# Kernel tuning notes

Measured on AMD Instinct MI355X. Metric: run time of the kernel, lower is better.

## Reference

```python
import jax, jax.numpy as jnp
import numpy as np

B, T, N_EMBD, HEAD = 4, 4096, 1024, 64


def setup_inputs() -> dict:
    key = jax.random.key(0)
    kx, kk, kq, kv = jax.random.split(key, 4)
    x = jax.random.normal(kx, (B, T, N_EMBD), dtype=jnp.float32)
    s = 1.0 / np.sqrt(N_EMBD)  # init scale so activations stay O(1)
    Wk = jax.random.normal(kk, (N_EMBD, HEAD), dtype=jnp.float32) * s
    Wq = jax.random.normal(kq, (N_EMBD, HEAD), dtype=jnp.float32) * s
    Wv = jax.random.normal(kv, (N_EMBD, HEAD), dtype=jnp.float32) * s
    return {"x": x, "Wk": Wk, "Wq": Wq, "Wv": Wv}


def reference(x, Wk, Wq, Wv):
    Bd, Td, C = x.shape
    k = jnp.einsum('btc,ch->bth', x, Wk)
    q = jnp.einsum('btc,ch->bth', x, Wq)
    v = jnp.einsum('btc,ch->bth', x, Wv)
    # scores scaled by C**-0.5 where C = n_embd (as in the source, not head_size)
    w = jnp.einsum('bth,bsh->bts', q, k) * (C ** -0.5)
    causal = jnp.tril(jnp.ones((Td, Td), dtype=bool))  # [T, T]
    w = jnp.where(causal, w, -jnp.inf)
    w = jax.nn.softmax(w, axis=-1)
    out = jnp.einsum('bts,bsh->bth', w, v)  # [B, T, head_size]
    return out
```

## Files before the change

kernel.cpp:

```cpp
#include <hip/hip_runtime.h>
#include <cmath>

#define NB 4
#define NT 4096
#define NC 1024
#define NH 64
#define SCALE 0.03125f
#define MFIX 3.0f
#define LOG2E 1.4426950408889634f
#define NSPLIT 12

typedef __attribute__((ext_vector_type(8))) short v8s;
typedef __attribute__((ext_vector_type(4))) float f32x4;

static __device__ __forceinline__ ushort f2bf(float x) {
    union { float f; uint u; } c; c.f = x;
    return (ushort)((c.u + 0x7FFF + ((c.u >> 16) & 1)) >> 16);
}
static __device__ __forceinline__ float bf2f(ushort h) {
    union { uint u; float f; } c; c.u = (uint)h << 16;
    return c.f;
}
static __device__ __forceinline__ uint pk2bf(float hi_f, float lo_f) {
    uint uh = __float_as_uint(hi_f) + 0x8000u;
    uint ul = __float_as_uint(lo_f) + 0x8000u;
    return __builtin_amdgcn_perm(uh, ul, 0x07060302u);
}

__global__ __launch_bounds__(256) void prep_kernel(
    const float* __restrict__ Wk, const float* __restrict__ Wq,
    const float* __restrict__ Wv, ushort* __restrict__ Wb)
{
    const int g    = blockIdx.x * 256 + threadIdx.x;
    const int lane = g & 63;
    const int kc   = (g >> 6) & 31;
    const int nt   = g >> 11;
    const int n    = nt * 16 + (lane & 15);
    const float* W = (n < 64) ? Wq : (n < 128) ? Wk : Wv;
    const int col  = n & 63;
    const int k0   = kc * 32 + ((lane >> 4) << 3);
    ushort t8[8];
    #pragma unroll
    for (int j = 0; j < 8; ++j)
        t8[j] = f2bf(W[(k0 + j) * 64 + col]);
    *(uint4*)(Wb + (size_t)g * 8) = *(const uint4*)t8;
}

#define PPAD 72

__global__ __launch_bounds__(256) void proj_kernel(
    const float* __restrict__ x, const ushort* __restrict__ Wb,
    ushort* __restrict__ qpack, ushort* __restrict__ kpack,
    ushort* __restrict__ vpack)
{
    __shared__ __align__(16) ushort As[2][16 * PPAD];
    __shared__ __align__(16) ushort Cs[16][200];

    const int tid  = threadIdx.x;
    const int w    = tid >> 6;
    const int lane = tid & 63;
    const int ln   = lane & 15;
    const int quad = lane >> 4;
    const long r0  = (long)blockIdx.x * 16;

    const int arow = tid >> 4, acol = (tid & 15) * 4;
    const float* xs = x + (r0 + arow) * NC + acol;

    const ushort* wb0 = Wb + (size_t)(w * 3 + 0) * 16384 + lane * 8;
    const ushort* wb1 = Wb + (size_t)(w * 3 + 1) * 16384 + lane * 8;
    const ushort* wb2 = Wb + (size_t)(w * 3 + 2) * 16384 + lane * 8;

    f32x4 acc[3];
    #pragma unroll
    for (int nt = 0; nt < 3; ++nt) acc[nt] = (f32x4){0.f,0.f,0.f,0.f};

    float4 f0 = *(const float4*)(xs);
    v8s b[3][2];
    b[0][0] = *(const v8s*)(wb0);       b[0][1] = *(const v8s*)(wb0 + 512);
    b[1][0] = *(const v8s*)(wb1);       b[1][1] = *(const v8s*)(wb1 + 512);
    b[2][0] = *(const v8s*)(wb2);       b[2][1] = *(const v8s*)(wb2 + 512);
    {
        uint2 p = { pk2bf(f0.y, f0.x), pk2bf(f0.w, f0.z) };
        *(uint2*)(&As[0][arow * PPAD + acol]) = p;
    }
    __syncthreads();

    int buf = 0;
    #pragma unroll
    for (int it = 0; it < 16; ++it) {
        float4 g0;
        v8s nb[3][2];
        if (it < 15) {
            const int k1 = (it + 1) * 64;
            g0 = *(const float4*)(xs + k1);
            const int off = (it + 1) * 1024;
            nb[0][0] = *(const v8s*)(wb0 + off); nb[0][1] = *(const v8s*)(wb0 + off + 512);
            nb[1][0] = *(const v8s*)(wb1 + off); nb[1][1] = *(const v8s*)(wb1 + off + 512);
            nb[2][0] = *(const v8s*)(wb2 + off); nb[2][1] = *(const v8s*)(wb2 + off + 512);
        }

        const ushort* ap = &As[buf][ln * PPAD + quad * 8];
        v8s a0 = *(const v8s*)(ap);
        v8s a1 = *(const v8s*)(ap + 32);
        #pragma unroll
        for (int nt = 0; nt < 3; ++nt) {
            acc[nt] = __builtin_amdgcn_mfma_f32_16x16x32_bf16(a0, b[nt][0], acc[nt], 0, 0, 0);
            acc[nt] = __builtin_amdgcn_mfma_f32_16x16x32_bf16(a1, b[nt][1], acc[nt], 0, 0, 0);
        }

        if (it < 15) {
            uint2 p = { pk2bf(g0.y, g0.x), pk2bf(g0.w, g0.z) };
            *(uint2*)(&As[buf ^ 1][arow * PPAD + acol]) = p;
            #pragma unroll
            for (int nt = 0; nt < 3; ++nt) {
                b[nt][0] = nb[nt][0];
                b[nt][1] = nb[nt][1];
            }
        }
        __syncthreads();
        buf ^= 1;
    }

    #pragma unroll
    for (int nt = 0; nt < 3; ++nt)
        #pragma unroll
        for (int r = 0; r < 4; ++r)
            Cs[quad * 4 + r][(w * 3 + nt) * 16 + ln] = f2bf(acc[nt][r]);
    __syncthreads();

    const int b_blk = (int)(r0 >> 12);
    const int t_loc = (int)(r0 & 4095);
    const int kt    = t_loc >> 6;
    const int qt16  = t_loc >> 4;
    const int kcb   = (t_loc >> 5) & 1;
    const int half  = (t_loc >> 4) & 1;

    if (tid < 128) {
        const int kc = tid >> 6, lp = tid & 63;
        const int lnp = lp & 15, qdp = lp >> 4;
        uint4 u = *(const uint4*)(&Cs[lnp][kc * 32 + qdp * 8]);
        size_t fid = ((size_t)(b_blk * 256 + qt16) * 2 + kc);
        *(uint4*)(qpack + fid * 512 + lp * 8) = u;
        const int td = tid >> 5, lp2 = tid & 31;
        const int ql = lp2 >> 4, lnv = lp2 & 15;
        ushort t8[8];
        #pragma unroll
        for (int j = 0; j < 8; ++j)
            t8[j] = Cs[ql * 8 + j][128 + td * 16 + lnv];
        size_t fv = ((size_t)(b_blk * 64 + kt) * 2 + kcb) * 4 + td;
        const int lane_g = (half * 2 + ql) * 16 + lnv;
        *(uint4*)(vpack + fv * 512 + lane_g * 8) = *(const uint4*)t8;
    } else {
        const int kc = (tid >> 6) & 1, lp = tid & 63;
        const int lnp = lp & 15, qdp = lp >> 4;
        uint4 u = *(const uint4*)(&Cs[lnp][64 + kc * 32 + qdp * 8]);
        size_t fid = ((size_t)(b_blk * 256 + qt16) * 2 + kc);
        *(uint4*)(kpack + fid * 512 + lp * 8) = u;
    }
}

#define LPAD 72

__global__ __launch_bounds__(256) void attn_kernel(
    const ushort* __restrict__ qpack, const ushort* __restrict__ kpack,
    const ushort* __restrict__ vpack, ushort* __restrict__ Op,
    float* __restrict__ Lp)
{
    __shared__ __align__(16) ushort Ps[4][32 * LPAD];

    const int id = blockIdx.x;
    const int qt = 31 - (id / 48);
    const int c  = (id % 48) >> 2;
    const int b  = id & 3;
    const int q0 = qt * 128;

    const int tid  = threadIdx.x;
    const int w    = tid >> 6;
    const int lane = tid & 63;
    const int ln   = lane & 15;
    const int quad = lane >> 4;
    const int qw0  = q0 + w * 32;
    const int qt16w = (qw0 >> 4);

    const ushort* qpb = qpack + (size_t)b * 256 * 2 * 512 + lane * 8;
    const ushort* kpb = kpack + (size_t)b * 64 * 8 * 512 + lane * 8;
    const ushort* vpb = vpack + (size_t)b * 64 * 8 * 512 + lane * 8;

    v8s qf[2][2];
    #pragma unroll
    for (int s = 0; s < 2; ++s) {
        qf[s][0] = *(const v8s*)(qpb + ((qt16w + s) * 2 + 0) * 512);
        qf[s][1] = *(const v8s*)(qpb + ((qt16w + s) * 2 + 1) * 512);
    }

    f32x4 o[2][4];
    #pragma unroll
    for (int s = 0; s < 2; ++s)
        #pragma unroll
        for (int td = 0; td < 4; ++td) o[s][td] = (f32x4){0.f,0.f,0.f,0.f};
    float l[2] = {0.f, 0.f};

    const int nkt   = 2 * qt + 2;
    const int cs    = (nkt + NSPLIT - 1) / NSPLIT;
    const int kt_lo = c * cs;
    const int kt_hi = min(nkt, kt_lo + cs);

    ushort* Pw = &Ps[w][0];

    for (int kt = kt_lo; kt < kt_hi; ++kt) {
        const ushort* kfb = kpb + (size_t)kt * 8 * 512;
        const ushort* vfb = vpb + (size_t)kt * 8 * 512;

        #pragma unroll
        for (int tk = 0; tk < 4; ++tk) {
            v8s kf0 = *(const v8s*)(kfb + (tk * 2 + 0) * 512);
            v8s kf1 = *(const v8s*)(kfb + (tk * 2 + 1) * 512);
            const int keybase = kt * 64 + tk * 16 + quad * 4;
            #pragma unroll
            for (int s = 0; s < 2; ++s) {
                f32x4 acc = (f32x4){0.f,0.f,0.f,0.f};
                acc = __builtin_amdgcn_mfma_f32_16x16x32_bf16(kf0, qf[s][0], acc, 0, 0, 0);
                acc = __builtin_amdgcn_mfma_f32_16x16x32_bf16(kf1, qf[s][1], acc, 0, 0, 0);
                const int qg = qw0 + s * 16 + ln;
                const bool needmask = (kt * 64 + 63) > (qw0 + s * 16);
                float p[4];
                #pragma unroll
                for (int r = 0; r < 4; ++r) {
                    float e = fmaf(acc[r], SCALE * LOG2E, -MFIX * LOG2E);
                    if (needmask && (keybase + r > qg)) e = -1e30f;
                    p[r] = __builtin_amdgcn_exp2f(e);
                    l[s] += p[r];
                }
                uint2 pw = { pk2bf(p[1], p[0]), pk2bf(p[3], p[2]) };
                *(uint2*)(&Pw[(s * 16 + ln) * LPAD + tk * 16 + quad * 4]) = pw;
            }
        }

        #pragma unroll
        for (int kc = 0; kc < 2; ++kc) {
            v8s vf[4];
            #pragma unroll
            for (int td = 0; td < 4; ++td)
                vf[td] = *(const v8s*)(vfb + (kc * 4 + td) * 512);
            #pragma unroll
            for (int s = 0; s < 2; ++s) {
                v8s pf = *(const v8s*)(&Pw[(s * 16 + ln) * LPAD + kc * 32 + quad * 8]);
                #pragma unroll
                for (int td = 0; td < 4; ++td)
                    o[s][td] = __builtin_amdgcn_mfma_f32_16x16x32_bf16(pf, vf[td], o[s][td], 0, 0, 0);
            }
        }
    }

    #pragma unroll
    for (int s = 0; s < 2; ++s) {
        l[s] += __shfl_xor(l[s], 16);
        l[s] += __shfl_xor(l[s], 32);
    }

    ushort* opc = Op + (size_t)c * NB * NT * NH + (size_t)b * NT * NH;
    float*  lpc = Lp + (size_t)c * NB * NT + (size_t)b * NT;
    #pragma unroll
    for (int s = 0; s < 2; ++s) {
        if (quad == 0) lpc[qw0 + s * 16 + ln] = l[s];
        #pragma unroll
        for (int r = 0; r < 4; ++r) {
            const int t = qw0 + s * 16 + quad * 4 + r;
            #pragma unroll
            for (int td = 0; td < 4; ++td)
                opc[(size_t)t * NH + td * 16 + ln] = f2bf(o[s][td][r]);
        }
    }
}

__global__ __launch_bounds__(256) void combine_kernel(
    const ushort* __restrict__ Op, const float* __restrict__ Lp,
    float* __restrict__ out)
{
    const size_t g4 = (size_t)blockIdx.x * 256 + threadIdx.x;
    const size_t h0 = (g4 & 15) * 4;
    const size_t bq = g4 >> 4;
    const size_t QN = (size_t)NB * NT;
    const size_t ON = QN * NH;
    float L = 0.f;
    float o0 = 0.f, o1 = 0.f, o2 = 0.f, o3 = 0.f;
    #pragma unroll
    for (int c = 0; c < NSPLIT; ++c) {
        L += Lp[(size_t)c * QN + bq];
        ushort4 u = *(const ushort4*)(Op + (size_t)c * ON + bq * NH + h0);
        o0 += bf2f(u.x); o1 += bf2f(u.y); o2 += bf2f(u.z); o3 += bf2f(u.w);
    }
    const float inv = 1.f / L;
    float4 r = { o0 * inv, o1 * inv, o2 * inv, o3 * inv };
    *(float4*)(out + bq * NH + h0) = r;
}

extern "C" void kernel_launch(void* const* d_in, const int* in_sizes, int n_in,
                              void* d_out, int out_size, void* d_ws, size_t ws_size,
                              hipStream_t stream)
{
    const float* x  = (const float*)d_in[0];
    const float* Wk = (const float*)d_in[1];
    const float* Wq = (const float*)d_in[2];
    const float* Wv = (const float*)d_in[3];
    float* out = (float*)d_out;

    char* wsb = (char*)d_ws;
    const size_t QE = (size_t)NB * NT * NH;
    ushort* qpack = (ushort*)wsb;
    ushort* kpack = qpack + QE;
    ushort* vpack = kpack + QE;
    ushort* Wb    = vpack + QE;
    ushort* Op    = (ushort*)(wsb + (8u << 20));
    float*  Lp    = (float*)(wsb + (40u << 20));

    prep_kernel<<<96, 256, 0, stream>>>(Wk, Wq, Wv, Wb);
    proj_kernel<<<NB * NT / 16, 256, 0, stream>>>(x, Wb, qpack, kpack, vpack);
    attn_kernel<<<32 * NSPLIT * NB, 256, 0, stream>>>(qpack, kpack, vpack, Op, Lp);
    combine_kernel<<<(int)(QE / 4 / 256), 256, 0, stream>>>(Op, Lp, out);
}
```

Baseline: 143.6 us.

## Double projection rows per block and store attention partials in fragment layout

The projection kernel now handles 32 rows per block instead of 16, so each loaded weight fragment feeds twice as many MFMAs and x loads are 8-wide. The attention kernel writes its partial outputs as packed bf16 in MFMA fragment order with vector stores, replacing scattered 2-byte stores. The combine kernel reads that fragment layout with vector loads and sums four L values at once. The trade-off is half as many projection blocks, which lowers parallelism, plus combine output writes that are now strided rather than float4.

```diff
diff --git a/kernel.cpp b/kernel.cpp
--- a/kernel.cpp
+++ b/kernel.cpp
@@ -9,6 +9,7 @@
 #define MFIX 3.0f
 #define LOG2E 1.4426950408889634f
 #define NSPLIT 12
+#define QE 1048576
 
 typedef __attribute__((ext_vector_type(8))) short v8s;
 typedef __attribute__((ext_vector_type(4))) float f32x4;
@@ -53,64 +54,73 @@
     ushort* __restrict__ qpack, ushort* __restrict__ kpack,
     ushort* __restrict__ vpack)
 {
-    __shared__ __align__(16) ushort As[2][16 * PPAD];
-    __shared__ __align__(16) ushort Cs[16][200];
+    __shared__ __align__(16) ushort As[2][32 * PPAD];
+    __shared__ __align__(16) ushort Cs[32][200];
 
     const int tid  = threadIdx.x;
     const int w    = tid >> 6;
     const int lane = tid & 63;
     const int ln   = lane & 15;
     const int quad = lane >> 4;
-    const long r0  = (long)blockIdx.x * 16;
-
-    const int arow = tid >> 4, acol = (tid & 15) * 4;
+    const long r0  = (long)blockIdx.x * 32;
+
+    const int arow = tid >> 3, acol = (tid & 7) * 8;
     const float* xs = x + (r0 + arow) * NC + acol;
 
     const ushort* wb0 = Wb + (size_t)(w * 3 + 0) * 16384 + lane * 8;
     const ushort* wb1 = Wb + (size_t)(w * 3 + 1) * 16384 + lane * 8;
     const ushort* wb2 = Wb + (size_t)(w * 3 + 2) * 16384 + lane * 8;
 
-    f32x4 acc[3];
-    #pragma unroll
-    for (int nt = 0; nt < 3; ++nt) acc[nt] = (f32x4){0.f,0.f,0.f,0.f};
+    f32x4 acc[2][3];
+    #pragma unroll
+    for (int s = 0; s < 2; ++s)
+        #pragma unroll
+        for (int nt = 0; nt < 3; ++nt) acc[s][nt] = (f32x4){0.f,0.f,0.f,0.f};
 
     float4 f0 = *(const float4*)(xs);
+    float4 f1 = *(const float4*)(xs + 4);
     v8s b[3][2];
     b[0][0] = *(const v8s*)(wb0);       b[0][1] = *(const v8s*)(wb0 + 512);
     b[1][0] = *(const v8s*)(wb1);       b[1][1] = *(const v8s*)(wb1 + 512);
     b[2][0] = *(const v8s*)(wb2);       b[2][1] = *(const v8s*)(wb2 + 512);
     {
-        uint2 p = { pk2bf(f0.y, f0.x), pk2bf(f0.w, f0.z) };
-        *(uint2*)(&As[0][arow * PPAD + acol]) = p;
+        uint4 p = { pk2bf(f0.y, f0.x), pk2bf(f0.w, f0.z),
+                    pk2bf(f1.y, f1.x), pk2bf(f1.w, f1.z) };
+        *(uint4*)(&As[0][arow * PPAD + acol]) = p;
     }
     __syncthreads();
 
     int buf = 0;
     #pragma unroll
     for (int it = 0; it < 16; ++it) {
-        float4 g0;
+        float4 g0, g1;
         v8s nb[3][2];
         if (it < 15) {
             const int k1 = (it + 1) * 64;
             g0 = *(const float4*)(xs + k1);
+            g1 = *(const float4*)(xs + k1 + 4);
             const int off = (it + 1) * 1024;
             nb[0][0] = *(const v8s*)(wb0 + off); nb[0][1] = *(const v8s*)(wb0 + off + 512);
             nb[1][0] = *(const v8s*)(wb1 + off); nb[1][1] = *(const v8s*)(wb1 + off + 512);
             nb[2][0] = *(const v8s*)(wb2 + off); nb[2][1] = *(const v8s*)(wb2 + off + 512);
         }
 
-        const ushort* ap = &As[buf][ln * PPAD + quad * 8];
-        v8s a0 = *(const v8s*)(ap);
-        v8s a1 = *(const v8s*)(ap + 32);
-        #pragma unroll
-        for (int nt = 0; nt < 3; ++nt) {
-            acc[nt] = __builtin_amdgcn_mfma_f32_16x16x32_bf16(a0, b[nt][0], acc[nt], 0, 0, 0);
-            acc[nt] = __builtin_amdgcn_mfma_f32_16x16x32_bf16(a1, b[nt][1], acc[nt], 0, 0, 0);
+        #pragma unroll
+        for (int s = 0; s < 2; ++s) {
+            const ushort* ap = &As[buf][(s * 16 + ln) * PPAD + quad * 8];
+            v8s a0 = *(const v8s*)(ap);
+            v8s a1 = *(const v8s*)(ap + 32);
+            #pragma unroll
+            for (int nt = 0; nt < 3; ++nt) {
+                acc[s][nt] = __builtin_amdgcn_mfma_f32_16x16x32_bf16(a0, b[nt][0], acc[s][nt], 0, 0, 0);
+                acc[s][nt] = __builtin_amdgcn_mfma_f32_16x16x32_bf16(a1, b[nt][1], acc[s][nt], 0, 0, 0);
+            }
         }
 
         if (it < 15) {
-            uint2 p = { pk2bf(g0.y, g0.x), pk2bf(g0.w, g0.z) };
-            *(uint2*)(&As[buf ^ 1][arow * PPAD + acol]) = p;
+            uint4 p = { pk2bf(g0.y, g0.x), pk2bf(g0.w, g0.z),
+                        pk2bf(g1.y, g1.x), pk2bf(g1.w, g1.z) };
+            *(uint4*)(&As[buf ^ 1][arow * PPAD + acol]) = p;
             #pragma unroll
             for (int nt = 0; nt < 3; ++nt) {
                 b[nt][0] = nb[nt][0];
@@ -122,40 +132,38 @@
     }
 
     #pragma unroll
-    for (int nt = 0; nt < 3; ++nt)
-        #pragma unroll
-        for (int r = 0; r < 4; ++r)
-            Cs[quad * 4 + r][(w * 3 + nt) * 16 + ln] = f2bf(acc[nt][r]);
+    for (int s = 0; s < 2; ++s)
+        #pragma unroll
+        for (int nt = 0; nt < 3; ++nt)
+            #pragma unroll
+            for (int r = 0; r < 4; ++r)
+                Cs[s * 16 + quad * 4 + r][(w * 3 + nt) * 16 + ln] = f2bf(acc[s][nt][r]);
     __syncthreads();
 
     const int b_blk = (int)(r0 >> 12);
     const int t_loc = (int)(r0 & 4095);
     const int kt    = t_loc >> 6;
-    const int qt16  = t_loc >> 4;
     const int kcb   = (t_loc >> 5) & 1;
-    const int half  = (t_loc >> 4) & 1;
-
-    if (tid < 128) {
-        const int kc = tid >> 6, lp = tid & 63;
+    const int qt16a = t_loc >> 4;
+
+    {
+        const int f = tid >> 6, sx = f >> 1, kc = f & 1, lp = tid & 63;
         const int lnp = lp & 15, qdp = lp >> 4;
-        uint4 u = *(const uint4*)(&Cs[lnp][kc * 32 + qdp * 8]);
-        size_t fid = ((size_t)(b_blk * 256 + qt16) * 2 + kc);
-        *(uint4*)(qpack + fid * 512 + lp * 8) = u;
-        const int td = tid >> 5, lp2 = tid & 31;
-        const int ql = lp2 >> 4, lnv = lp2 & 15;
+        const size_t fid = ((size_t)(b_blk * 256 + qt16a + sx) * 2 + kc);
+        uint4 uq = *(const uint4*)(&Cs[sx * 16 + lnp][kc * 32 + qdp * 8]);
+        *(uint4*)(qpack + fid * 512 + lp * 8) = uq;
+        uint4 uk = *(const uint4*)(&Cs[sx * 16 + lnp][64 + kc * 32 + qdp * 8]);
+        *(uint4*)(kpack + fid * 512 + lp * 8) = uk;
+    }
+    {
+        const int td = tid >> 6, lp = tid & 63;
+        const int lnv = lp & 15, qg = lp >> 4;
         ushort t8[8];
         #pragma unroll
         for (int j = 0; j < 8; ++j)
-            t8[j] = Cs[ql * 8 + j][128 + td * 16 + lnv];
-        size_t fv = ((size_t)(b_blk * 64 + kt) * 2 + kcb) * 4 + td;
-        const int lane_g = (half * 2 + ql) * 16 + lnv;
-        *(uint4*)(vpack + fv * 512 + lane_g * 8) = *(const uint4*)t8;
-    } else {
-        const int kc = (tid >> 6) & 1, lp = tid & 63;
-        const int lnp = lp & 15, qdp = lp >> 4;
-        uint4 u = *(const uint4*)(&Cs[lnp][64 + kc * 32 + qdp * 8]);
-        size_t fid = ((size_t)(b_blk * 256 + qt16) * 2 + kc);
-        *(uint4*)(kpack + fid * 512 + lp * 8) = u;
+            t8[j] = Cs[qg * 8 + j][128 + td * 16 + lnv];
+        const size_t fv = ((size_t)(b_blk * 64 + kt) * 2 + kcb) * 4 + td;
+        *(uint4*)(vpack + fv * 512 + lp * 8) = *(const uint4*)t8;
     }
 }
 
@@ -258,17 +266,16 @@
         l[s] += __shfl_xor(l[s], 32);
     }
 
-    ushort* opc = Op + (size_t)c * NB * NT * NH + (size_t)b * NT * NH;
-    float*  lpc = Lp + (size_t)c * NB * NT + (size_t)b * NT;
+    float* lpc = Lp + (size_t)c * NB * NT + (size_t)b * NT;
+    const size_t obase = (((size_t)c * NB + b) * 32 + qt) * 4 + w;
     #pragma unroll
     for (int s = 0; s < 2; ++s) {
         if (quad == 0) lpc[qw0 + s * 16 + ln] = l[s];
         #pragma unroll
-        for (int r = 0; r < 4; ++r) {
-            const int t = qw0 + s * 16 + quad * 4 + r;
-            #pragma unroll
-            for (int td = 0; td < 4; ++td)
-                opc[(size_t)t * NH + td * 16 + ln] = f2bf(o[s][td][r]);
+        for (int td = 0; td < 4; ++td) {
+            uint2 pw = { pk2bf(o[s][td][1], o[s][td][0]),
+                         pk2bf(o[s][td][3], o[s][td][2]) };
+            *(uint2*)(Op + (((obase * 2 + s) * 4 + td) * 256 + lane * 4)) = pw;
         }
     }
 }
@@ -277,22 +284,34 @@
     const ushort* __restrict__ Op, const float* __restrict__ Lp,
     float* __restrict__ out)
 {
-    const size_t g4 = (size_t)blockIdx.x * 256 + threadIdx.x;
-    const size_t h0 = (g4 & 15) * 4;
-    const size_t bq = g4 >> 4;
+    const uint g   = blockIdx.x * 256 + threadIdx.x;
+    const int lane = g & 63, ln = lane & 15, quad = lane >> 4;
+    const int td   = (g >> 6) & 3;
+    const int s    = (g >> 8) & 1;
+    const int w    = (g >> 9) & 3;
+    const int qt   = (g >> 11) & 31;
+    const int b    = (g >> 16) & 3;
     const size_t QN = (size_t)NB * NT;
-    const size_t ON = QN * NH;
-    float L = 0.f;
+
+    const int q0 = qt * 128 + w * 32 + s * 16 + quad * 4;
+    const size_t foff = ((((((size_t)b * 32 + qt) * 4 + w) * 2 + s) * 4 + td) * 256)
+                        + lane * 4;
+
     float o0 = 0.f, o1 = 0.f, o2 = 0.f, o3 = 0.f;
+    float L0 = 0.f, L1 = 0.f, L2 = 0.f, L3 = 0.f;
     #pragma unroll
     for (int c = 0; c < NSPLIT; ++c) {
-        L += Lp[(size_t)c * QN + bq];
-        ushort4 u = *(const ushort4*)(Op + (size_t)c * ON + bq * NH + h0);
-        o0 += bf2f(u.x); o1 += bf2f(u.y); o2 += bf2f(u.z); o3 += bf2f(u.w);
-    }
-    const float inv = 1.f / L;
-    float4 r = { o0 * inv, o1 * inv, o2 * inv, o3 * inv };
-    *(float4*)(out + bq * NH + h0) = r;
+        uint2 u = *(const uint2*)(Op + (size_t)c * QE + foff);
+        o0 += bf2f((ushort)(u.x & 0xffff)); o1 += bf2f((ushort)(u.x >> 16));
+        o2 += bf2f((ushort)(u.y & 0xffff)); o3 += bf2f((ushort)(u.y >> 16));
+        float4 Lv = *(const float4*)(Lp + (size_t)c * QN + (size_t)b * NT + q0);
+        L0 += Lv.x; L1 += Lv.y; L2 += Lv.z; L3 += Lv.w;
+    }
+    float* ob = out + ((size_t)b * NT + q0) * NH + td * 16 + ln;
+    ob[0]   = o0 / L0;
+    ob[64]  = o1 / L1;
+    ob[128] = o2 / L2;
+    ob[192] = o3 / L3;
 }
 
 extern "C" void kernel_launch(void* const* d_in, const int* in_sizes, int n_in,
@@ -306,7 +325,6 @@
     float* out = (float*)d_out;
 
     char* wsb = (char*)d_ws;
-    const size_t QE = (size_t)NB * NT * NH;
     ushort* qpack = (ushort*)wsb;
     ushort* kpack = qpack + QE;
     ushort* vpack = kpack + QE;
@@ -315,7 +333,7 @@
     float*  Lp    = (float*)(wsb + (40u << 20));
 
     prep_kernel<<<96, 256, 0, stream>>>(Wk, Wq, Wv, Wb);
-    proj_kernel<<<NB * NT / 16, 256, 0, stream>>>(x, Wb, qpack, kpack, vpack);
+    proj_kernel<<<NB * NT / 32, 256, 0, stream>>>(x, Wb, qpack, kpack, vpack);
     attn_kernel<<<32 * NSPLIT * NB, 256, 0, stream>>>(qpack, kpack, vpack, Op, Lp);
     combine_kernel<<<(int)(QE / 4 / 256), 256, 0, stream>>>(Op, Lp, out);
 }
```

New measurement: 134.8 us. 1.07x faster.
